# Kernel tuning notes

Measured on AMD Instinct MI355X. Metric: run time of the kernel, lower is better.

## Reference

```python
import jax, jax.numpy as jnp
import numpy as np

N_EMBED = 1024
N_HEAD = 16
D = N_EMBED // N_HEAD
B, T = 2, 2048
EPS = 1e-5


def _layer_norm(x, w, b):
    mu = jnp.mean(x, axis=-1, keepdims=True)
    var = jnp.mean(jnp.square(x - mu), axis=-1, keepdims=True)
    return (x - mu) * jax.lax.rsqrt(var + EPS) * w + b


def setup_inputs() -> dict:
    key = jax.random.key(0)
    ks = jax.random.split(key, 13)
    E = N_EMBED
    s_attn = 1.0 / np.sqrt(E)
    s_fc = 1.0 / np.sqrt(E)
    s_proj = 1.0 / np.sqrt(4 * E)
    return {
        "x": jax.random.normal(ks[0], (B, T, E), jnp.float32),
        "ln1_w": jnp.ones((E,), jnp.float32),
        "ln1_b": jnp.ones((E,), jnp.float32),
        "w_qkv": jax.random.normal(ks[1], (E, 3 * E), jnp.float32) * s_attn,
        "b_qkv": jax.random.normal(ks[2], (3 * E,), jnp.float32) * 0.02,
        "w_o": jax.random.normal(ks[3], (E, E), jnp.float32) * s_attn,
        "b_o": jax.random.normal(ks[4], (E,), jnp.float32) * 0.02,
        "ln2_w": jnp.ones((E,), jnp.float32),
        "ln2_b": jnp.ones((E,), jnp.float32),
        "w_fc": jax.random.normal(ks[5], (E, 4 * E), jnp.float32) * s_fc,
        "b_fc": jax.random.normal(ks[6], (4 * E,), jnp.float32) * 0.02,
        "w_proj": jax.random.normal(ks[7], (4 * E, E), jnp.float32) * s_proj,
        "b_proj": jax.random.normal(ks[8], (E,), jnp.float32) * 0.02,
    }


def reference(x, ln1_w, ln1_b, w_qkv, b_qkv, w_o, b_o, ln2_w, ln2_b, w_fc, b_fc, w_proj, b_proj):
    Bb, Tt, E = x.shape
    # --- attention branch ---
    h = _layer_norm(x, ln1_w, ln1_b)
    qkv = h @ w_qkv + b_qkv                         # [B,T,3E]
    q, k, v = jnp.split(qkv, 3, axis=-1)
    q = q.reshape(Bb, Tt, N_HEAD, D).transpose(0, 2, 1, 3)  # [B,H,T,D]
    k = k.reshape(Bb, Tt, N_HEAD, D).transpose(0, 2, 1, 3)
    v = v.reshape(Bb, Tt, N_HEAD, D).transpose(0, 2, 1, 3)
    scale = 1.0 / np.sqrt(D)
    a = scale * jnp.einsum("bhqd,bhkd->bhqk", q, k)  # [B,H,T,T]
    causal = jnp.tril(jnp.ones((Tt, Tt), bool))
    a = jnp.where(causal, a, -jnp.inf)
    a = jax.nn.softmax(a, axis=-1)
    y = jnp.einsum("bhqk,bhkd->bhqd", a, v)          # [B,H,T,D]
    y = y.transpose(0, 2, 1, 3).reshape(Bb, Tt, E)
    y = y @ w_o + b_o
    x = x + y
    # --- MLP branch ---
    h = _layer_norm(x, ln2_w, ln2_b)
    h = jax.nn.gelu(h @ w_fc + b_fc, approximate=False)
    h = h @ w_proj + b_proj
    return x + h
```

## Files before the change

### kernel.cpp

```cpp
#include <hip/hip_runtime.h>
#include <cstdint>
#include <cstddef>

#define E 1024
#define TT 2048
#define NB 2
#define NH 16
#define HD 64

using u16 = unsigned short;
using bf16x8 = __attribute__((ext_vector_type(8))) __bf16;
using floatx4 = __attribute__((ext_vector_type(4))) float;
using s16x4 = __attribute__((ext_vector_type(4))) short;

__device__ __forceinline__ float b2f(u16 u) {
  unsigned int x = ((unsigned int)u) << 16;
  float f;
  __builtin_memcpy(&f, &x, 4);
  return f;
}
__device__ __forceinline__ u16 f2b(float f) {
  unsigned int x;
  __builtin_memcpy(&x, &f, 4);
  x += 0x7fffu + ((x >> 16) & 1u);
  return (u16)(x >> 16);
}
__device__ __forceinline__ u16 f2b_fast(float f) {
  unsigned int x;
  float g = f * 1.001953125f;
  __builtin_memcpy(&x, &g, 4);
  return (u16)(x >> 16);
}

__device__ __forceinline__ void async16(const u16* g, u16* l) {
  __builtin_amdgcn_global_load_lds(
      (const __attribute__((address_space(1))) unsigned int*)g,
      (__attribute__((address_space(3))) unsigned int*)l, 16, 0, 0);
}

__device__ __forceinline__ floatx4 mfma32(bf16x8 a, bf16x8 b, floatx4 c) {
  return __builtin_amdgcn_mfma_f32_16x16x32_bf16(a, b, c, 0, 0, 0);
}

__device__ __forceinline__ floatx4 mfma16(s16x4 a, s16x4 b, floatx4 c) {
#if defined(__HIP_DEVICE_COMPILE__)
  return __builtin_amdgcn_mfma_f32_16x16x16bf16_1k(a, b, c, 0, 0, 0);
#else
  return c;
#endif
}

__global__ __launch_bounds__(256) void wconv_all(
    const float* __restrict__ w0, const float* __restrict__ w1,
    const float* __restrict__ w2, const float* __restrict__ w3,
    u16* __restrict__ o0, u16* __restrict__ o1, u16* __restrict__ o2,
    u16* __restrict__ o3) {
  __shared__ float tile[32][33];
  const int t = blockIdx.x;
  const float* w;
  u16* o;
  int K, N, nx, ti;
  if (t < 3072) { w = w0; o = o0; K = 1024; N = 3072; nx = 96; ti = t; }
  else if (t < 4096) { w = w1; o = o1; K = 1024; N = 1024; nx = 32; ti = t - 3072; }
  else if (t < 8192) { w = w2; o = o2; K = 1024; N = 4096; nx = 128; ti = t - 4096; }
  else { w = w3; o = o3; K = 4096; N = 1024; nx = 32; ti = t - 8192; }
  const int n0 = (ti % nx) * 32, k0 = (ti / nx) * 32;
  const int tx = threadIdx.x, ty = threadIdx.y;
#pragma unroll
  for (int i = 0; i < 32; i += 8)
    tile[ty + i][tx] = w[(size_t)(k0 + ty + i) * N + (n0 + tx)];
  __syncthreads();
  const int ft = ty * 32 + tx;
  const int nl = ft >> 3, ch = ft & 7;
  ushort4 pk;
  pk.x = f2b(tile[ch * 4 + 0][nl]);
  pk.y = f2b(tile[ch * 4 + 1][nl]);
  pk.z = f2b(tile[ch * 4 + 2][nl]);
  pk.w = f2b(tile[ch * 4 + 3][nl]);
  *(ushort4*)(o + (size_t)(n0 + nl) * K + k0 + ch * 4) = pk;
}

__global__ __launch_bounds__(256) void ln_kernel(const float* __restrict__ x,
                                                 const float* __restrict__ w,
                                                 const float* __restrict__ bvec,
                                                 u16* __restrict__ outb) {
  const int row = blockIdx.x;
  const int t = threadIdx.x;
  const float4 v = ((const float4*)(x + (size_t)row * E))[t];
  float s1 = v.x + v.y + v.z + v.w;
  float s2 = v.x * v.x + v.y * v.y + v.z * v.z + v.w * v.w;
#pragma unroll
  for (int off = 32; off > 0; off >>= 1) {
    s1 += __shfl_down(s1, off);
    s2 += __shfl_down(s2, off);
  }
  __shared__ float r1[4], r2[4];
  if ((t & 63) == 0) { r1[t >> 6] = s1; r2[t >> 6] = s2; }
  __syncthreads();
  s1 = r1[0] + r1[1] + r1[2] + r1[3];
  s2 = r2[0] + r2[1] + r2[2] + r2[3];
  const float mean = s1 * (1.f / E);
  const float var = s2 * (1.f / E) - mean * mean;
  const float rstd = rsqrtf(var + 1e-5f);
  const float4 wv = ((const float4*)w)[t];
  const float4 bv = ((const float4*)bvec)[t];
  const u16 o0 = f2b((v.x - mean) * rstd * wv.x + bv.x);
  const u16 o1 = f2b((v.y - mean) * rstd * wv.y + bv.y);
  const u16 o2 = f2b((v.z - mean) * rstd * wv.z + bv.z);
  const u16 o3 = f2b((v.w - mean) * rstd * wv.w + bv.w);
  uint2 pk;
  pk.x = (unsigned)o0 | ((unsigned)o1 << 16);
  pk.y = (unsigned)o2 | ((unsigned)o3 << 16);
  ((uint2*)(outb + (size_t)row * E))[t] = pk;
}

template <int MODE, int ROWS>
__global__ __launch_bounds__(512) void gemm_bt(const u16* __restrict__ A,
                                               const u16* __restrict__ BT,
                                               const float* __restrict__ bias,
                                               const float* __restrict__ res,
                                               void* __restrict__ outp,
                                               int M, int N, int K) {
  constexpr int NJ = (ROWS == 256) ? 4 : 2;
  __shared__ __align__(16) u16 As[3][ROWS * 32];
  __shared__ __align__(16) u16 Bs[3][128 * 32];
  const int tid = threadIdx.x;
  const int wave = tid >> 6, lane = tid & 63;

  const int gx = gridDim.x, gy = gridDim.y;
  const int L = blockIdx.y * gx + blockIdx.x;
  const int xc = L & 7, wi = L >> 3;
  const int cpg = gx >> 2;
  const int rpg = gy >> 1;
  const int bxs = (xc >> 1) * cpg + (wi % cpg);
  const int bys = (xc & 1) * rpg + (wi / cpg);

  const int row0 = bys * ROWS, col0 = bxs * 128;
  const int wm = (ROWS == 256) ? (wave & 3) * 64 : (wave & 1) * 64;
  const int wn = (ROWS == 256) ? (wave >> 2) * 64 : (wave >> 1) * 32;
  const int r = lane & 15, qd = lane >> 4;

  floatx4 acc[4][NJ];
#pragma unroll
  for (int i = 0; i < 4; i++)
#pragma unroll
    for (int j = 0; j < NJ; j++) acc[i][j] = (floatx4){0.f, 0.f, 0.f, 0.f};

  const int cA0 = tid, cA1 = tid + 512, cB = tid;
  const u16* ApA = A + (size_t)(row0 + (cA0 >> 2)) * K + (cA0 & 3) * 8;
  const u16* ApB = A + (size_t)(row0 + (cA1 >> 2)) * K + (cA1 & 3) * 8;
  const u16* Bp = BT + (size_t)(col0 + (cB >> 2)) * K + (cB & 3) * 8;

  auto stage = [&](int kt, u16* Asb, u16* Bsb) {
    async16(ApA + kt, Asb + cA0 * 8);
    if (ROWS == 256) async16(ApB + kt, Asb + cA1 * 8);
    async16(Bp + kt, Bsb + cB * 8);
  };
  auto compute = [&](const u16* Asb, const u16* Bsb) {
    bf16x8 af[4], bfr[NJ];
#pragma unroll
    for (int i = 0; i < 4; i++)
      af[i] = *(const bf16x8*)&Asb[(wm + i * 16 + r) * 32 + qd * 8];
#pragma unroll
    for (int j = 0; j < NJ; j++)
      bfr[j] = *(const bf16x8*)&Bsb[(wn + j * 16 + r) * 32 + qd * 8];
#pragma unroll
    for (int i = 0; i < 4; i++)
#pragma unroll
      for (int j = 0; j < NJ; j++)
        acc[i][j] = mfma32(af[i], bfr[j], acc[i][j]);
  };

  const int nIter = K >> 5;
  stage(0, As[0], Bs[0]);
  stage(32, As[1], Bs[1]);
  for (int tt = 0; tt < nIter; tt += 3) {
#pragma unroll
    for (int d = 0; d < 3; d++) {
      const int t = tt + d;
      if (t >= nIter) break;
      if (t + 1 < nIter) {
        if (ROWS == 256)
          asm volatile("s_waitcnt vmcnt(3)" ::: "memory");
        else
          asm volatile("s_waitcnt vmcnt(2)" ::: "memory");
      } else {
        asm volatile("s_waitcnt vmcnt(0)" ::: "memory");
      }
      asm volatile("s_barrier" ::: "memory");
      if (t + 2 < nIter) {
        const int sd = (d + 2 >= 3) ? d - 1 : d + 2;
        stage((t + 2) * 32, As[sd], Bs[sd]);
      }
      compute(As[d], Bs[d]);
    }
  }

#pragma unroll
  for (int i = 0; i < 4; i++) {
#pragma unroll
    for (int j = 0; j < NJ; j++) {
      const int col = col0 + wn + j * 16 + r;
      const float bc = bias[col];
      if (MODE == 3) {
        u16* base = (u16*)outp;
        const int rowb = row0 + wm + i * 16 + qd * 4;
        if (col < 2048) {
          const size_t cb =
              (col < 1024) ? (size_t)col : ((size_t)4096 * 1024 + (col - 1024));
#pragma unroll
          for (int rr = 0; rr < 4; rr++)
            base[cb + (size_t)(rowb + rr) * 1024] = f2b(acc[i][j][rr] + bc);
        } else {
          ushort4 pk;
          pk.x = f2b(acc[i][j][0] + bc);
          pk.y = f2b(acc[i][j][1] + bc);
          pk.z = f2b(acc[i][j][2] + bc);
          pk.w = f2b(acc[i][j][3] + bc);
          *(ushort4*)(base + (size_t)8 * 1024 * 1024 +
                      (size_t)(col - 2048) * 4096 + rowb) = pk;
        }
      } else {
#pragma unroll
        for (int rr = 0; rr < 4; rr++) {
          const int row = row0 + wm + i * 16 + qd * 4 + rr;
          const float v = acc[i][j][rr] + bc;
          const size_t idx = (size_t)row * N + col;
          if (MODE == 0) {
            ((u16*)outp)[idx] = f2b(v);
          } else if (MODE == 1) {
            ((float*)outp)[idx] = v + res[idx];
          } else {
            const float z = 1.5957691216f * v * (1.f + 0.044715f * v * v);
            const float g = v / (1.f + __expf(-z));
            ((u16*)outp)[idx] = f2b(g);
          }
        }
      }
    }
  }
}

__global__ __launch_bounds__(512) void gemm_ks(const u16* __restrict__ A,
                                               const u16* __restrict__ BT,
                                               const float* __restrict__ bias,
                                               const float* __restrict__ res,
                                               float* __restrict__ outp,
                                               int M, int N, int K) {
  __shared__ __align__(16) u16 As[4][2][128 * 32];
  __shared__ __align__(16) u16 Bs[4][2][128 * 32];
  const int tid = threadIdx.x;
  const int wave = tid >> 6, lane = tid & 63;

  const int gx = gridDim.x, gy = gridDim.y;
  const int L = blockIdx.y * gx + blockIdx.x;
  const int xc = L & 7, wi = L >> 3;
  const int cpg = gx >> 2, rpg = gy >> 1;
  const int bxs = (xc >> 1) * cpg + (wi % cpg);
  const int bys = (xc & 1) * rpg + (wi / cpg);

  const int row0 = bys * 128, col0 = bxs * 128;
  const int kg = wave >> 2;
  const int wm = (wave & 1) * 64, wn = ((wave >> 1) & 1) * 64;
  const int r = lane & 15, qd = lane >> 4;

  floatx4 acc[4][4];
#pragma unroll
  for (int i = 0; i < 4; i++)
#pragma unroll
    for (int j = 0; j < 4; j++) acc[i][j] = (floatx4){0.f, 0.f, 0.f, 0.f};

  const int arow = tid >> 2, aslot = (tid & 3) * 8;
  const u16* Ap = A + (size_t)(row0 + arow) * K + aslot;
  const u16* Bp = BT + (size_t)(col0 + arow) * K + aslot;

  auto stage = [&](int s, int d) {
    const int k0 = s * 64;
    async16(Ap + k0, &As[d][0][tid * 8]);
    async16(Ap + k0 + 32, &As[d][1][tid * 8]);
    async16(Bp + k0, &Bs[d][0][tid * 8]);
    async16(Bp + k0 + 32, &Bs[d][1][tid * 8]);
  };
  auto compute = [&](int d) {
    bf16x8 af[4], bfr[4];
#pragma unroll
    for (int i = 0; i < 4; i++)
      af[i] = *(const bf16x8*)&As[d][kg][(wm + i * 16 + r) * 32 + qd * 8];
#pragma unroll
    for (int j = 0; j < 4; j++)
      bfr[j] = *(const bf16x8*)&Bs[d][kg][(wn + j * 16 + r) * 32 + qd * 8];
#pragma unroll
    for (int i = 0; i < 4; i++)
#pragma unroll
      for (int j = 0; j < 4; j++)
        acc[i][j] = mfma32(af[i], bfr[j], acc[i][j]);
  };

  const int nT = K >> 6;
  stage(0, 0);
  stage(1, 1);
  stage(2, 2);
  for (int tt = 0; tt < nT; tt += 4) {
#pragma unroll
    for (int d = 0; d < 4; d++) {
      const int t = tt + d;
      const int rem = nT - 1 - t;
      if (rem >= 2)
        asm volatile("s_waitcnt vmcnt(8)" ::: "memory");
      else if (rem == 1)
        asm volatile("s_waitcnt vmcnt(4)" ::: "memory");
      else
        asm volatile("s_waitcnt vmcnt(0)" ::: "memory");
      asm volatile("s_barrier" ::: "memory");
      if (t + 3 < nT) stage(t + 3, (d + 3) & 3);
      compute(d);
    }
  }

  __syncthreads();
  float* S = (float*)&As[0][0][0];
  const int p = wave & 3;
  floatx4* W = (floatx4*)S + p * 1024 + lane;
  if (kg == 1) {
#pragma unroll
    for (int i = 0; i < 4; i++)
#pragma unroll
      for (int j = 0; j < 4; j++) W[(i * 4 + j) * 64] = acc[i][j];
  }
  __syncthreads();
  if (kg == 0) {
#pragma unroll
    for (int i = 0; i < 4; i++) {
#pragma unroll
      for (int j = 0; j < 4; j++) {
        const floatx4 w2 = W[(i * 4 + j) * 64];
        const int col = col0 + wn + j * 16 + r;
        const float bc = bias[col];
#pragma unroll
        for (int rr = 0; rr < 4; rr++) {
          const int row = row0 + wm + i * 16 + qd * 4 + rr;
          const size_t idx = (size_t)row * N + col;
          outp[idx] = acc[i][j][rr] + w2[rr] + bc + res[idx];
        }
      }
    }
  }
}

__global__ __launch_bounds__(512, 4) void attn_mfma(const u16* __restrict__ qb,
                                                    const u16* __restrict__ kb,
                                                    const u16* __restrict__ vtb,
                                                    u16* __restrict__ y) {
  const int bx = blockIdx.x;
  const int h = blockIdx.y, b = blockIdx.z;
  const int qt = b ? (15 - bx) : bx;
  const int tid = threadIdx.x;
  const int wave = tid >> 6, lane = tid & 63;
  const int quad = lane >> 4, r = lane & 15;
  const int wq = wave & 3;
  const int kvh = wave >> 2;

  __shared__ __align__(16) u16 lds[2 * 128 * 64 + 2 * 64 * 128];
  u16* KsB = lds;
  u16* VsB = lds + 2 * 128 * 64;

  const float C = 0.125f * 1.44269504f;
  const int qbase = qt * 128 + wq * 32;

  bf16x8 qf[2][2];
#pragma unroll
  for (int f = 0; f < 2; f++) {
    const u16* qp = qb + ((size_t)b * TT + qbase + f * 16 + r) * E + h * 64;
#pragma unroll
    for (int kh = 0; kh < 2; kh++) {
      union { bf16x8 v; u16 u[8]; } tmp;
#pragma unroll
      for (int j = 0; j < 8; j++) tmp.u[j] = f2b(b2f(qp[kh * 32 + quad * 8 + j]) * C);
      qf[f][kh] = tmp.v;
    }
  }

  floatx4 o[2][4];
#pragma unroll
  for (int f = 0; f < 2; f++)
#pragma unroll
    for (int i = 0; i < 4; i++) o[f][i] = (floatx4){0.f, 0.f, 0.f, 0.f};
  float lsum[2] = {0.f, 0.f};
  const bool mgt[4] = {(quad * 4 + 0) > r, (quad * 4 + 1) > r,
                       (quad * 4 + 2) > r, (quad * 4 + 3) > r};

  auto stageKV = [&](int it, int bi) {
    const int k0 = it * 128;
    u16* Kd = KsB + bi * (128 * 64);
    u16* Vd = VsB + bi * (64 * 128);
#pragma unroll
    for (int i = 0; i < 2; i++) {
      const int c = tid + i * 512;
      const int key = c >> 3, dc = (c & 7) ^ (key & 7);
      async16(kb + ((size_t)b * TT + k0 + key) * E + h * 64 + dc * 8, Kd + c * 8);
    }
#pragma unroll
    for (int i = 0; i < 2; i++) {
      const int c = tid + i * 512;
      const int d = c >> 4, kc = (c & 15) ^ (d & 15);
      async16(vtb + (size_t)(h * 64 + d) * (NB * TT) + b * TT + k0 + kc * 8,
              Vd + c * 8);
    }
  };

  const int nIter = qt + 1;
  stageKV(0, 0);
  for (int it = 0; it < nIter; it++) {
    if (it + 1 < nIter) {
      stageKV(it + 1, (it + 1) & 1);
      asm volatile("s_waitcnt vmcnt(4)" ::: "memory");
    } else {
      asm volatile("s_waitcnt vmcnt(0)" ::: "memory");
    }
    asm volatile("s_barrier" ::: "memory");
    const u16* Kb = KsB + (it & 1) * (128 * 64);
    const u16* Vb = VsB + (it & 1) * (64 * 128);
    const int k0 = it * 128;
    const int relA = (qbase - k0) >> 4;
    const int kTop = (relA + 1 < 7) ? (relA + 1) : 7;

#pragma unroll
    for (int kk = 0; kk < 4; kk++) {
      const int ks = kvh * 4 + kk;
      if (ks <= kTop) {
        const int key = ks * 16 + r, kx = key & 7;
        const bf16x8 kf0 = *(const bf16x8*)&Kb[key * 64 + (quad ^ kx) * 8];
        const bf16x8 kf1 = *(const bf16x8*)&Kb[key * 64 + ((4 + quad) ^ kx) * 8];
        floatx4 s0 = (floatx4){0.f, 0.f, 0.f, 0.f};
        s0 = mfma32(kf0, qf[0][0], s0);
        s0 = mfma32(kf1, qf[0][1], s0);
        floatx4 s1 = (floatx4){0.f, 0.f, 0.f, 0.f};
        s1 = mfma32(kf0, qf[1][0], s1);
        s1 = mfma32(kf1, qf[1][1], s1);

        s16x4 vf[4];
#pragma unroll
        for (int dsub = 0; dsub < 4; dsub++) {
          const int d = dsub * 16 + r;
          vf[dsub] = *(const s16x4*)&Vb[d * 128 + ((2 * ks + (quad >> 1)) ^ r) * 8 +
                                        (quad & 1) * 4];
        }

#pragma unroll
        for (int f = 0; f < 2; f++) {
          const floatx4 sv = (f == 0) ? s0 : s1;
          const int rel = relA + f;
          if (ks <= rel) {
            float p0 = exp2f(sv[0]);
            float p1 = exp2f(sv[1]);
            float p2 = exp2f(sv[2]);
            float p3 = exp2f(sv[3]);
            if (ks == rel) {
              if (mgt[0]) p0 = 0.f;
              if (mgt[1]) p1 = 0.f;
              if (mgt[2]) p2 = 0.f;
              if (mgt[3]) p3 = 0.f;
            }
            lsum[f] += p0 + p1 + p2 + p3;
            s16x4 pk;
            pk[0] = (short)f2b_fast(p0);
            pk[1] = (short)f2b_fast(p1);
            pk[2] = (short)f2b_fast(p2);
            pk[3] = (short)f2b_fast(p3);
#pragma unroll
            for (int dsub = 0; dsub < 4; dsub++)
              o[f][dsub] = mfma16(pk, vf[dsub], o[f][dsub]);
          }
        }
      }
    }
    asm volatile("s_barrier" ::: "memory");
  }

  floatx4* W = (floatx4*)(float*)lds + wq * 576 + lane;
  if (kvh == 1) {
#pragma unroll
    for (int f = 0; f < 2; f++)
#pragma unroll
      for (int dsub = 0; dsub < 4; dsub++) W[(f * 4 + dsub) * 64] = o[f][dsub];
    W[8 * 64] = (floatx4){lsum[0], lsum[1], 0.f, 0.f};
  }
  __syncthreads();
  if (kvh == 0) {
    const floatx4 ls2 = W[8 * 64];
#pragma unroll
    for (int f = 0; f < 2; f++) {
      float lv = lsum[f] + ((f == 0) ? ls2[0] : ls2[1]);
      lv += __shfl_xor(lv, 16);
      lv += __shfl_xor(lv, 32);
      float linv[4];
#pragma unroll
      for (int rr = 0; rr < 4; rr++) linv[rr] = 1.f / __shfl(lv, quad * 4 + rr);
#pragma unroll
      for (int dsub = 0; dsub < 4; dsub++) {
        const floatx4 o2 = W[(f * 4 + dsub) * 64];
#pragma unroll
        for (int rr = 0; rr < 4; rr++) {
          const size_t row = (size_t)b * TT + qbase + f * 16 + quad * 4 + rr;
          y[row * E + h * 64 + dsub * 16 + r] =
              f2b((o[f][dsub][rr] + o2[rr]) * linv[rr]);
        }
      }
    }
  }
}

extern "C" void kernel_launch(void* const* d_in, const int* in_sizes, int n_in,
                              void* d_out, int out_size, void* d_ws, size_t ws_size,
                              hipStream_t stream) {
  (void)in_sizes; (void)n_in; (void)out_size; (void)ws_size;
  const float* x      = (const float*)d_in[0];
  const float* ln1w   = (const float*)d_in[1];
  const float* ln1b   = (const float*)d_in[2];
  const float* w_qkv  = (const float*)d_in[3];
  const float* b_qkv  = (const float*)d_in[4];
  const float* w_o    = (const float*)d_in[5];
  const float* b_o    = (const float*)d_in[6];
  const float* ln2w   = (const float*)d_in[7];
  const float* ln2b   = (const float*)d_in[8];
  const float* w_fc   = (const float*)d_in[9];
  const float* b_fc   = (const float*)d_in[10];
  const float* w_proj = (const float*)d_in[11];
  const float* b_proj = (const float*)d_in[12];
  float* out = (float*)d_out;

  char* p = (char*)d_ws;
  u16* wT_qkv  = (u16*)p; p += (size_t)3072 * 1024 * 2;
  u16* wT_o    = (u16*)p; p += (size_t)1024 * 1024 * 2;
  u16* wT_fc   = (u16*)p; p += (size_t)4096 * 1024 * 2;
  u16* wT_proj = (u16*)p; p += (size_t)1024 * 4096 * 2;
  u16* hbuf    = (u16*)p; p += (size_t)4096 * 1024 * 2;
  u16* qkvb    = (u16*)p; p += (size_t)4096 * 3072 * 2;
  float* x2    = (float*)p; p += (size_t)4096 * 1024 * 4;
  u16* gbuf    = (u16*)p; p += (size_t)4096 * 4096 * 2;

  u16* qb  = qkvb;
  u16* kb  = qkvb + (size_t)4096 * 1024;
  u16* vtb = qkvb + (size_t)8 * 1024 * 1024;

  wconv_all<<<12288, dim3(32, 8), 0, stream>>>(w_qkv, w_o, w_fc, w_proj,
                                               wT_qkv, wT_o, wT_fc, wT_proj);

  ln_kernel<<<4096, 256, 0, stream>>>(x, ln1w, ln1b, hbuf);
  gemm_bt<3, 256><<<dim3(3072 / 128, 4096 / 256), 512, 0, stream>>>(
      hbuf, wT_qkv, b_qkv, nullptr, qkvb, 4096, 3072, 1024);
  attn_mfma<<<dim3(16, NH, NB), 512, 0, stream>>>(qb, kb, vtb, hbuf);
  gemm_ks<<<dim3(1024 / 128, 4096 / 128), 512, 0, stream>>>(
      hbuf, wT_o, b_o, x, x2, 4096, 1024, 1024);
  ln_kernel<<<4096, 256, 0, stream>>>(x2, ln2w, ln2b, hbuf);
  gemm_bt<2, 256><<<dim3(4096 / 128, 4096 / 256), 512, 0, stream>>>(
      hbuf, wT_fc, b_fc, nullptr, gbuf, 4096, 4096, 1024);
  gemm_ks<<<dim3(1024 / 128, 4096 / 128), 512, 0, stream>>>(
      gbuf, wT_proj, b_proj, x2, out, 4096, 1024, 4096);
}
```

Measured before the change: 322.2 us.

## Shrink split-K GEMM tile to 64x128 with swizzled LDS and 3-stage pipeline

The split-K GEMM used for the output and MLP projections now uses 64-row tiles instead of 128, doubling the grid to 512 blocks on the N=1024 GEMMs. LDS is laid out as 64-wide k rows with an XOR swizzle to avoid bank conflicts, and the pipeline drops from 4 stages to 3 to cut LDS use, with launch bounds requesting 4 blocks per CU. The aim is more blocks for better CU fill and occupancy, at the cost of less data reuse per tile and more global loads of the B operand.

```diff
diff --git a/kernel.cpp b/kernel.cpp
--- a/kernel.cpp
+++ b/kernel.cpp
@@ -241,14 +241,15 @@
   }
 }
 
-__global__ __launch_bounds__(512) void gemm_ks(const u16* __restrict__ A,
-                                               const u16* __restrict__ BT,
-                                               const float* __restrict__ bias,
-                                               const float* __restrict__ res,
-                                               float* __restrict__ outp,
-                                               int M, int N, int K) {
-  __shared__ __align__(16) u16 As[4][2][128 * 32];
-  __shared__ __align__(16) u16 Bs[4][2][128 * 32];
+__global__ __launch_bounds__(512, 4) void gemm_ks(const u16* __restrict__ A,
+                                                  const u16* __restrict__ BT,
+                                                  const float* __restrict__ bias,
+                                                  const float* __restrict__ res,
+                                                  float* __restrict__ outp,
+                                                  int M, int N, int K) {
+  __shared__ __align__(16) u16 lds[3 * (64 * 64 + 128 * 64)];
+  u16* AsB = lds;
+  u16* BsB = lds + 3 * 64 * 64;
   const int tid = threadIdx.x;
   const int wave = tid >> 6, lane = tid & 63;
 
@@ -259,38 +260,46 @@
   const int bxs = (xc >> 1) * cpg + (wi % cpg);
   const int bys = (xc & 1) * rpg + (wi / cpg);
 
-  const int row0 = bys * 128, col0 = bxs * 128;
+  const int row0 = bys * 64, col0 = bxs * 128;
   const int kg = wave >> 2;
-  const int wm = (wave & 1) * 64, wn = ((wave >> 1) & 1) * 64;
+  const int wm = (wave & 1) * 32, wn = ((wave >> 1) & 1) * 64;
   const int r = lane & 15, qd = lane >> 4;
 
-  floatx4 acc[4][4];
-#pragma unroll
-  for (int i = 0; i < 4; i++)
+  floatx4 acc[2][4];
+#pragma unroll
+  for (int i = 0; i < 2; i++)
 #pragma unroll
     for (int j = 0; j < 4; j++) acc[i][j] = (floatx4){0.f, 0.f, 0.f, 0.f};
 
-  const int arow = tid >> 2, aslot = (tid & 3) * 8;
-  const u16* Ap = A + (size_t)(row0 + arow) * K + aslot;
-  const u16* Bp = BT + (size_t)(col0 + arow) * K + aslot;
+  const int arow = tid >> 3;
+  const int aks = (tid & 7) ^ (arow & 7);
+  const u16* Ap = A + (size_t)(row0 + arow) * K + aks * 8;
+  const u16* Bp1 = BT + (size_t)(col0 + arow) * K + aks * 8;
+  const u16* Bp2 = BT + (size_t)(col0 + 64 + arow) * K + aks * 8;
 
   auto stage = [&](int s, int d) {
     const int k0 = s * 64;
-    async16(Ap + k0, &As[d][0][tid * 8]);
-    async16(Ap + k0 + 32, &As[d][1][tid * 8]);
-    async16(Bp + k0, &Bs[d][0][tid * 8]);
-    async16(Bp + k0 + 32, &Bs[d][1][tid * 8]);
+    async16(Ap + k0, AsB + d * (64 * 64) + tid * 8);
+    async16(Bp1 + k0, BsB + d * (128 * 64) + tid * 8);
+    async16(Bp2 + k0, BsB + d * (128 * 64) + (512 + tid) * 8);
   };
   auto compute = [&](int d) {
-    bf16x8 af[4], bfr[4];
-#pragma unroll
-    for (int i = 0; i < 4; i++)
-      af[i] = *(const bf16x8*)&As[d][kg][(wm + i * 16 + r) * 32 + qd * 8];
-#pragma unroll
-    for (int j = 0; j < 4; j++)
-      bfr[j] = *(const bf16x8*)&Bs[d][kg][(wn + j * 16 + r) * 32 + qd * 8];
-#pragma unroll
-    for (int i = 0; i < 4; i++)
+    const u16* Ad = AsB + d * (64 * 64);
+    const u16* Bd = BsB + d * (128 * 64);
+    const int c = kg * 4 + qd;
+    bf16x8 af[2], bfr[4];
+#pragma unroll
+    for (int i = 0; i < 2; i++) {
+      const int row = wm + i * 16 + r;
+      af[i] = *(const bf16x8*)&Ad[row * 64 + (c ^ (row & 7)) * 8];
+    }
+#pragma unroll
+    for (int j = 0; j < 4; j++) {
+      const int row = wn + j * 16 + r;
+      bfr[j] = *(const bf16x8*)&Bd[row * 64 + (c ^ (row & 7)) * 8];
+    }
+#pragma unroll
+    for (int i = 0; i < 2; i++)
 #pragma unroll
       for (int j = 0; j < 4; j++)
         acc[i][j] = mfma32(af[i], bfr[j], acc[i][j]);
@@ -299,38 +308,36 @@
   const int nT = K >> 6;
   stage(0, 0);
   stage(1, 1);
-  stage(2, 2);
-  for (int tt = 0; tt < nT; tt += 4) {
-#pragma unroll
-    for (int d = 0; d < 4; d++) {
+  for (int tt = 0; tt < nT; tt += 3) {
+#pragma unroll
+    for (int d = 0; d < 3; d++) {
       const int t = tt + d;
-      const int rem = nT - 1 - t;
-      if (rem >= 2)
-        asm volatile("s_waitcnt vmcnt(8)" ::: "memory");
-      else if (rem == 1)
-        asm volatile("s_waitcnt vmcnt(4)" ::: "memory");
+      if (t >= nT) break;
+      if (t + 1 < nT)
+        asm volatile("s_waitcnt vmcnt(3)" ::: "memory");
       else
         asm volatile("s_waitcnt vmcnt(0)" ::: "memory");
       asm volatile("s_barrier" ::: "memory");
-      if (t + 3 < nT) stage(t + 3, (d + 3) & 3);
+      if (t + 2 < nT) {
+        const int sd = (d + 2 >= 3) ? d - 1 : d + 2;
+        stage(t + 2, sd);
+      }
       compute(d);
     }
   }
 
   __syncthreads();
-  float* S = (float*)&As[0][0][0];
-  const int p = wave & 3;
-  floatx4* W = (floatx4*)S + p * 1024 + lane;
+  floatx4* W = (floatx4*)lds + (wave & 3) * 512 + lane;
   if (kg == 1) {
 #pragma unroll
-    for (int i = 0; i < 4; i++)
+    for (int i = 0; i < 2; i++)
 #pragma unroll
       for (int j = 0; j < 4; j++) W[(i * 4 + j) * 64] = acc[i][j];
   }
   __syncthreads();
   if (kg == 0) {
 #pragma unroll
-    for (int i = 0; i < 4; i++) {
+    for (int i = 0; i < 2; i++) {
 #pragma unroll
       for (int j = 0; j < 4; j++) {
         const floatx4 w2 = W[(i * 4 + j) * 64];
@@ -550,11 +557,11 @@
   gemm_bt<3, 256><<<dim3(3072 / 128, 4096 / 256), 512, 0, stream>>>(
       hbuf, wT_qkv, b_qkv, nullptr, qkvb, 4096, 3072, 1024);
   attn_mfma<<<dim3(16, NH, NB), 512, 0, stream>>>(qb, kb, vtb, hbuf);
-  gemm_ks<<<dim3(1024 / 128, 4096 / 128), 512, 0, stream>>>(
+  gemm_ks<<<dim3(1024 / 128, 4096 / 64), 512, 0, stream>>>(
       hbuf, wT_o, b_o, x, x2, 4096, 1024, 1024);
   ln_kernel<<<4096, 256, 0, stream>>>(x2, ln2w, ln2b, hbuf);
   gemm_bt<2, 256><<<dim3(4096 / 128, 4096 / 256), 512, 0, stream>>>(
       hbuf, wT_fc, b_fc, nullptr, gbuf, 4096, 4096, 1024);
-  gemm_ks<<<dim3(1024 / 128, 4096 / 128), 512, 0, stream>>>(
+  gemm_ks<<<dim3(1024 / 128, 4096 / 64), 512, 0, stream>>>(
       gbuf, wT_proj, b_proj, x2, out, 4096, 1024, 4096);
 }
```

New measurement: 310.1 us. 1.04x faster.
